# Optimization experiments

Hardware: AMD Instinct MI355X
Metric: run time of the kernel (lower is better)

The kernel has to match this reference:

```python
import jax, jax.numpy as jnp
import numpy as np

NEG_SLOPE = 0.2

def _gat_conv(x, W, att_src, att_dst, bias, src, dst, n_nodes):
    # x: [N, F_in], W: [F_in, F_out], att_*: [F_out], bias: [F_out]
    h = x @ W                                   # [N, F_out]
    a_src = h @ att_src                         # [N]
    a_dst = h @ att_dst                         # [N]
    e = a_src[src] + a_dst[dst]                 # [E]
    e = jnp.where(e > 0, e, NEG_SLOPE * e)      # LeakyReLU
    # segment softmax over incoming edges of each destination node
    m = jax.ops.segment_max(e, dst, num_segments=n_nodes)
    ex = jnp.exp(e - m[dst])
    denom = jax.ops.segment_sum(ex, dst, num_segments=n_nodes)
    alpha = ex / denom[dst]                     # [E]
    msg = alpha[:, None] * h[src]               # [E, F_out]
    out = jax.ops.segment_sum(msg, dst, num_segments=n_nodes)
    return out + bias

def setup_inputs() -> dict:
    key = jax.random.key(0)
    ks = jax.random.split(key, 12)
    N, E, F_in, H, F_out = 50000, 800000, 128, 128, 128
    def glorot(k, shape):
        lim = float(np.sqrt(6.0 / sum(shape))) if len(shape) > 1 else float(np.sqrt(6.0 / shape[0]))
        return jax.random.uniform(k, shape, jnp.float32, -lim, lim)
    return {
        "x": jax.random.normal(ks[0], (N, F_in), jnp.float32),
        "edge_index": jax.random.randint(ks[1], (2, E), 0, N, jnp.int64),
        "W1": glorot(ks[2], (F_in, H)),
        "att_src1": glorot(ks[3], (H,)),
        "att_dst1": glorot(ks[4], (H,)),
        "b1": jnp.zeros((H,), jnp.float32),
        "W2": glorot(ks[5], (H, F_out)),
        "att_src2": glorot(ks[6], (F_out,)),
        "att_dst2": glorot(ks[7], (F_out,)),
        "b2": jnp.zeros((F_out,), jnp.float32),
    }

def reference(x, edge_index, W1, att_src1, att_dst1, b1, W2, att_src2, att_dst2, b2):
    n_nodes = x.shape[0]
    # add self loops (PyG GATConv default)
    loops = jnp.arange(n_nodes, dtype=edge_index.dtype)
    src = jnp.concatenate([edge_index[0], loops])
    dst = jnp.concatenate([edge_index[1], loops])
    h = _gat_conv(x, W1, att_src1, att_dst1, b1, src, dst, n_nodes)
    h = jax.nn.relu(h)
    h = _gat_conv(h, W2, att_src2, att_dst2, b2, src, dst, n_nodes)
    return jax.nn.relu(h)
```

## Files before the change

kernel.cpp:

```cpp
#include <hip/hip_runtime.h>
#include <cstdint>

#define NEG_SLOPE 0.2f
#define F 128

#define BKT_SHIFT 7
#define BKT_SIZE  128
#define NBK_PAD   512
#define CHUNK     4096
#define EPT       8
#define CAP       3072

typedef unsigned short u16;
typedef unsigned int u32;
typedef float float8_t __attribute__((ext_vector_type(8)));
typedef float float4_t __attribute__((ext_vector_type(4)));
typedef short short8_t __attribute__((ext_vector_type(8)));

__device__ inline u16 f2bf(float f) {
    u32 u = __float_as_uint(f);
    u32 r = u + 0x7fffu + ((u >> 16) & 1u);
    return (u16)(r >> 16);
}
__device__ inline float bflo(u32 v) { return __uint_as_float(v << 16); }
__device__ inline float bfhi(u32 v) { return __uint_as_float(v & 0xffff0000u); }

__device__ inline void prep_unit(const float* __restrict__ W, u16* __restrict__ Wt, int u) {
    int frag = u >> 6, lane = u & 63;
    int K0 = frag >> 3, nt = frag & 7;
    int kbase = K0 * 32 + (lane >> 4) * 8;
    int n = nt * 16 + (lane & 15);
    u32 w[4];
    #pragma unroll
    for (int p = 0; p < 4; ++p) {
        u16 e0 = f2bf(W[(size_t)(kbase + 2 * p) * F + n]);
        u16 e1 = f2bf(W[(size_t)(kbase + 2 * p + 1) * F + n]);
        w[p] = (u32)e0 | ((u32)e1 << 16);
    }
    uint4 o; o.x = w[0]; o.y = w[1]; o.z = w[2]; o.w = w[3];
    ((uint4*)Wt)[u] = o;
}

__global__ void __launch_bounds__(512) scatter_prep_kernel(const int* __restrict__ ei, int E, int tot,
                                                           int* __restrict__ bucketCursor,
                                                           u32* __restrict__ pairs,
                                                           const float* __restrict__ W1, u16* __restrict__ Wt1,
                                                           const float* __restrict__ W2, u16* __restrict__ Wt2,
                                                           int nScatBlocks) {
    if ((int)blockIdx.x >= nScatBlocks) {
        int pb = blockIdx.x - nScatBlocks;
        int u = (pb & 3) * 512 + threadIdx.x;
        if (pb < 4) prep_unit(W1, Wt1, u);
        else        prep_unit(W2, Wt2, u);
        return;
    }
    __shared__ int hist[NBK_PAD], excl[NBK_PAD], lcur[NBK_PAD], runb[NBK_PAD];
    __shared__ u32 stage[CHUNK];
    __shared__ u16 bktid[CHUNK];
    int tid = threadIdx.x;
    hist[tid] = 0;
    __syncthreads();
    int base = blockIdx.x * CHUNK;
    int chunkCnt = min(CHUNK, tot - base);
    int rs[EPT], rd[EPT];
    int w = base + tid * EPT;
    if (w + EPT <= E) {
        int4 s0 = *(const int4*)&ei[w];
        int4 s1 = *(const int4*)&ei[w + 4];
        int4 d0 = *(const int4*)&ei[E + w];
        int4 d1 = *(const int4*)&ei[E + w + 4];
        rs[0] = s0.x; rs[1] = s0.y; rs[2] = s0.z; rs[3] = s0.w;
        rs[4] = s1.x; rs[5] = s1.y; rs[6] = s1.z; rs[7] = s1.w;
        rd[0] = d0.x; rd[1] = d0.y; rd[2] = d0.z; rd[3] = d0.w;
        rd[4] = d1.x; rd[5] = d1.y; rd[6] = d1.z; rd[7] = d1.w;
        #pragma unroll
        for (int i = 0; i < EPT; ++i) atomicAdd(&hist[rd[i] >> BKT_SHIFT], 1);
    } else {
        #pragma unroll
        for (int i = 0; i < EPT; ++i) {
            int e = w + i;
            rd[i] = -1;
            if (e < tot) {
                int s, d;
                if (e < E) { s = ei[e]; d = ei[E + e]; } else { s = e - E; d = s; }
                rs[i] = s; rd[i] = d;
                atomicAdd(&hist[d >> BKT_SHIFT], 1);
            }
        }
    }
    __syncthreads();
    int v = hist[tid];
    excl[tid] = v;
    __syncthreads();
    for (int o = 1; o < NBK_PAD; o <<= 1) {
        int u = (tid >= o) ? excl[tid - o] : 0;
        __syncthreads();
        excl[tid] += u;
        __syncthreads();
    }
    int ex = excl[tid] - v;
    __syncthreads();
    excl[tid] = ex;
    lcur[tid] = ex;
    if (v > 0) runb[tid] = tid * CAP + atomicAdd(&bucketCursor[tid], v);
    __syncthreads();
    #pragma unroll
    for (int i = 0; i < EPT; ++i) {
        if (rd[i] >= 0) {
            int b = rd[i] >> BKT_SHIFT;
            int pos = atomicAdd(&lcur[b], 1);
            stage[pos] = ((u32)rs[i] << BKT_SHIFT) | (u32)(rd[i] & (BKT_SIZE - 1));
            bktid[pos] = (u16)b;
        }
    }
    __syncthreads();
    for (int j = tid; j < chunkCnt; j += 512) {
        int b = (int)bktid[j];
        size_t idx = (size_t)runb[b] + (j - excl[b]);
        if (idx < (size_t)(b + 1) * CAP)
            pairs[idx] = stage[j];
    }
}

__global__ void __launch_bounds__(512) bucket_scan_kernel(const int* __restrict__ bucketCursor,
                                                          int* __restrict__ bucketStart) {
    __shared__ int sc[NBK_PAD];
    int t = threadIdx.x;
    int v = min(bucketCursor[t], CAP);
    sc[t] = v;
    __syncthreads();
    for (int o = 1; o < NBK_PAD; o <<= 1) {
        int u = (t >= o) ? sc[t - o] : 0;
        __syncthreads();
        sc[t] += u;
        __syncthreads();
    }
    bucketStart[t] = sc[t] - v;
    if (t == NBK_PAD - 1) bucketStart[NBK_PAD] = sc[t];
}

__device__ void build_body(const u32* __restrict__ pairs, const int* __restrict__ bucketStart,
                           int* __restrict__ row_ptr, int* __restrict__ csr,
                           int N, int tot, int b, char* smem) {
    u32* stage  = (u32*)smem;
    int* sorted = (int*)(smem + CAP * 4);
    int* hist   = (int*)(smem + CAP * 8);
    int* pfx    = (int*)(smem + CAP * 8 + 512);
    int* cur    = (int*)(smem + CAP * 8 + 1024);
    int tid = threadIdx.x;
    size_t srcb = (size_t)b * CAP;
    int dstb = bucketStart[b];
    int cnt = bucketStart[b + 1] - dstb;
    if (tid < BKT_SIZE) hist[tid] = 0;
    __syncthreads();
    for (int j = tid; j < cnt; j += 256) {
        u32 p = pairs[srcb + j];
        stage[j] = p;
        atomicAdd(&hist[p & (BKT_SIZE - 1)], 1);
    }
    __syncthreads();
    if (tid < BKT_SIZE) pfx[tid] = hist[tid];
    __syncthreads();
    for (int o = 1; o < BKT_SIZE; o <<= 1) {
        int u = 0;
        if (tid < BKT_SIZE && tid >= o) u = pfx[tid - o];
        __syncthreads();
        if (tid < BKT_SIZE) pfx[tid] += u;
        __syncthreads();
    }
    if (tid < BKT_SIZE) {
        int ex = pfx[tid] - hist[tid];
        cur[tid] = ex;
        int d = b * BKT_SIZE + tid;
        if (d < N) row_ptr[d] = dstb + ex;
    }
    __syncthreads();
    for (int j = tid; j < cnt; j += 256) {
        u32 p = stage[j];
        int pos = atomicAdd(&cur[p & (BKT_SIZE - 1)], 1);
        sorted[pos] = (int)(p >> BKT_SHIFT);
    }
    __syncthreads();
    for (int j = tid; j < cnt; j += 256) csr[(size_t)dstb + j] = sorted[j];
    if (b == 0 && tid == 0) row_ptr[N] = tot;
}

template<int IN_BF16>
__device__ void gemm_body(const void* __restrict__ in, const u16* __restrict__ Wt,
                          const float* __restrict__ att_s, const float* __restrict__ att_d,
                          u16* __restrict__ h, float* __restrict__ asrc, float* __restrict__ adst,
                          int N, int gblk, u16* wlds) {
    int tid = threadIdx.x;
    {
        const uint4* src = (const uint4*)Wt;
        uint4* dst = (uint4*)wlds;
        #pragma unroll
        for (int i = 0; i < 8; ++i) dst[tid + i * 256] = src[tid + i * 256];
    }
    __syncthreads();
    int wave = tid >> 6, lane = tid & 63;
    int li = lane & 15, grp = lane >> 4;
    int rowBase = (gblk * 4 + wave) * 16;
    if (rowBase >= N) return;
    int row = rowBase + li;
    if (row > N - 1) row = N - 1;

    short8_t b[4];
    if (IN_BF16) {
        const u16* xp = (const u16*)in + (size_t)row * F + grp * 8;
        #pragma unroll
        for (int K0 = 0; K0 < 4; ++K0)
            b[K0] = *(const short8_t*)(xp + K0 * 32);
    } else {
        const float* xp = (const float*)in + (size_t)row * F + grp * 8;
        #pragma unroll
        for (int K0 = 0; K0 < 4; ++K0) {
            float8_t xv = *(const float8_t*)(xp + K0 * 32);
            short8_t t;
            #pragma unroll
            for (int i = 0; i < 8; ++i) t[i] = (short)f2bf(xv[i]);
            b[K0] = t;
        }
    }

    float4_t acc[8];
    #pragma unroll
    for (int nt = 0; nt < 8; ++nt) acc[nt] = (float4_t){0.f, 0.f, 0.f, 0.f};
    #pragma unroll
    for (int nt = 0; nt < 8; ++nt) {
        #pragma unroll
        for (int K0 = 0; K0 < 4; ++K0) {
            short8_t a = *(const short8_t*)&wlds[((K0 * 8 + nt) * 64 + lane) * 8];
            acc[nt] = __builtin_amdgcn_mfma_f32_16x16x32_bf16(a, b[K0], acc[nt], 0, 0, 0);
        }
    }

    u16* hr = h + (size_t)row * F + grp * 4;
    #pragma unroll
    for (int nt = 0; nt < 8; ++nt) {
        u32 lo = (u32)f2bf(acc[nt][0]) | ((u32)f2bf(acc[nt][1]) << 16);
        u32 hi = (u32)f2bf(acc[nt][2]) | ((u32)f2bf(acc[nt][3]) << 16);
        uint2 st; st.x = lo; st.y = hi;
        *(uint2*)(hr + (size_t)nt * 16) = st;
    }

    float rs = 0.f, rd = 0.f;
    #pragma unroll
    for (int nt = 0; nt < 8; ++nt) {
        float4 a4 = *(const float4*)(att_s + nt * 16 + grp * 4);
        float4 d4 = *(const float4*)(att_d + nt * 16 + grp * 4);
        rs += acc[nt][0] * a4.x + acc[nt][1] * a4.y + acc[nt][2] * a4.z + acc[nt][3] * a4.w;
        rd += acc[nt][0] * d4.x + acc[nt][1] * d4.y + acc[nt][2] * d4.z + acc[nt][3] * d4.w;
    }
    rs += __shfl_xor(rs, 16); rs += __shfl_xor(rs, 32);
    rd += __shfl_xor(rd, 16); rd += __shfl_xor(rd, 32);
    if (grp == 0) { asrc[row] = rs; adst[row] = rd; }
}

template<int IN_BF16>
__global__ void __launch_bounds__(256) gemm_mfma_kernel(const void* __restrict__ in,
    const u16* __restrict__ Wt, const float* __restrict__ att_s, const float* __restrict__ att_d,
    u16* __restrict__ h, float* __restrict__ asrc, float* __restrict__ adst, int N)
{
    __shared__ u16 wlds[16384];
    gemm_body<IN_BF16>(in, Wt, att_s, att_d, h, asrc, adst, N, blockIdx.x, wlds);
}

__global__ void __launch_bounds__(256) build_gemm_kernel(
    const u32* __restrict__ pairs, const int* __restrict__ bucketStart,
    int* __restrict__ row_ptr, int* __restrict__ csr, int N, int tot,
    const float* __restrict__ x, const u16* __restrict__ Wt,
    const float* __restrict__ att_s, const float* __restrict__ att_d,
    u16* __restrict__ h, float* __restrict__ asrc, float* __restrict__ adst, int NBK)
{
    __shared__ __align__(16) char smem[32768];
    if ((int)blockIdx.x < NBK) {
        build_body(pairs, bucketStart, row_ptr, csr, N, tot, blockIdx.x, smem);
    } else {
        gemm_body<0>(x, Wt, att_s, att_d, h, asrc, adst, N, blockIdx.x - NBK, (u16*)smem);
    }
}

template<int U>
__device__ __forceinline__ void gfma(const uint4* __restrict__ h4, int lane, int s, float p, int t,
                                     float (&acc)[8]) {
    int ss[U]; float pp[U]; uint4 vv[U];
    #pragma unroll
    for (int i = 0; i < U; ++i) { ss[i] = __shfl(s, t + i, 16); pp[i] = __shfl(p, t + i, 16); }
    #pragma unroll
    for (int i = 0; i < U; ++i) vv[i] = h4[(size_t)ss[i] * 16 + lane];
    #pragma unroll
    for (int i = 0; i < U; ++i) {
        acc[0] = fmaf(pp[i], bflo(vv[i].x), acc[0]);
        acc[1] = fmaf(pp[i], bfhi(vv[i].x), acc[1]);
        acc[2] = fmaf(pp[i], bflo(vv[i].y), acc[2]);
        acc[3] = fmaf(pp[i], bfhi(vv[i].y), acc[3]);
        acc[4] = fmaf(pp[i], bflo(vv[i].z), acc[4]);
        acc[5] = fmaf(pp[i], bfhi(vv[i].z), acc[5]);
        acc[6] = fmaf(pp[i], bflo(vv[i].w), acc[6]);
        acc[7] = fmaf(pp[i], bfhi(vv[i].w), acc[7]);
    }
}

template<int OUT_BF16>
__global__ void __launch_bounds__(256) aggregate_kernel(
    const u16* __restrict__ h, const float* __restrict__ asrc, const float* __restrict__ adst,
    const int* __restrict__ row_ptr, const int* __restrict__ csr,
    const float* __restrict__ bias, void* __restrict__ out, int N)
{
    int gid = blockIdx.x * 16 + (threadIdx.x >> 4);
    if (gid >= N) return;
    int lane = threadIdx.x & 15;
    int start = row_ptr[gid];
    int deg = row_ptr[gid + 1] - start;
    float ad = adst[gid];

    const uint4* h4 = (const uint4*)h;
    float denom = 0.f;
    float acc[8] = {0.f, 0.f, 0.f, 0.f, 0.f, 0.f, 0.f, 0.f};

    int c0 = 0;
    int cnt = min(16, deg);
    int s = 0; float a = 0.f;
    if (lane < cnt) { s = csr[start + lane]; a = asrc[s]; }
    for (;;) {
        float p = 0.f;
        if (lane < cnt) {
            float e = a + ad;
            e = (e > 0.f) ? e : NEG_SLOPE * e;
            p = __expf(fminf(e, 70.f));
        }
        denom += p;

        int nc0 = c0 + 16;
        int ncnt = min(16, deg - nc0);
        int s2 = 0; float a2 = 0.f;
        if (nc0 < deg && lane < ncnt) { s2 = csr[start + nc0 + lane]; a2 = asrc[s2]; }

        int t = 0;
        for (; t + 8 <= cnt; t += 8) gfma<8>(h4, lane, s, p, t, acc);
        for (; t + 4 <= cnt; t += 4) gfma<4>(h4, lane, s, p, t, acc);
        for (; t < cnt; ++t)         gfma<1>(h4, lane, s, p, t, acc);

        if (nc0 >= deg) break;
        c0 = nc0; cnt = ncnt; s = s2; a = a2;
    }

    #pragma unroll
    for (int o = 1; o < 16; o <<= 1) denom += __shfl_xor(denom, o);
    float inv = 1.0f / denom;
    const float* bp = bias + lane * 8;
    float r[8];
    #pragma unroll
    for (int j = 0; j < 8; ++j) {
        float v = fmaf(acc[j], inv, bp[j]);
        r[j] = v > 0.f ? v : 0.f;
    }
    if (OUT_BF16) {
        u32 w[4];
        #pragma unroll
        for (int p2 = 0; p2 < 4; ++p2)
            w[p2] = (u32)f2bf(r[2 * p2]) | ((u32)f2bf(r[2 * p2 + 1]) << 16);
        uint4 st; st.x = w[0]; st.y = w[1]; st.z = w[2]; st.w = w[3];
        ((uint4*)out)[(size_t)gid * 16 + lane] = st;
    } else {
        float4 o0 = make_float4(r[0], r[1], r[2], r[3]);
        float4 o1 = make_float4(r[4], r[5], r[6], r[7]);
        ((float4*)out)[(size_t)gid * 32 + lane * 2]     = o0;
        ((float4*)out)[(size_t)gid * 32 + lane * 2 + 1] = o1;
    }
}

static inline size_t align_up(size_t v, size_t a) { return (v + a - 1) & ~(a - 1); }

extern "C" void kernel_launch(void* const* d_in, const int* in_sizes, int n_in,
                              void* d_out, int out_size, void* d_ws, size_t ws_size,
                              hipStream_t stream) {
    const float* x   = (const float*)d_in[0];
    const int*   ei  = (const int*)d_in[1];
    const float* W1  = (const float*)d_in[2];
    const float* as1 = (const float*)d_in[3];
    const float* ad1 = (const float*)d_in[4];
    const float* b1  = (const float*)d_in[5];
    const float* W2  = (const float*)d_in[6];
    const float* as2 = (const float*)d_in[7];
    const float* ad2 = (const float*)d_in[8];
    const float* b2  = (const float*)d_in[9];

    int N = in_sizes[0] / F;
    int E = in_sizes[1] / 2;
    int tot = E + N;

    char* ws = (char*)d_ws;
    size_t off = 0;
    #define ALLOC(type, name, count)                                    \
        type* name = (type*)(ws + off);                                  \
        off = align_up(off + (size_t)(count) * sizeof(type), 256);
    ALLOC(u16,   h,       (size_t)N * F);
    ALLOC(u16,   out1,    (size_t)N * F);
    ALLOC(float, asrc,    N);
    ALLOC(float, adst,    N);
    ALLOC(int,   row_ptr, N + 4);
    ALLOC(int,   csr,     tot);
    ALLOC(u32,   pairs,   (size_t)NBK_PAD * CAP);
    ALLOC(int,   bucketStart,  NBK_PAD + 1);
    ALLOC(int,   bucketCursor, NBK_PAD);
    ALLOC(u16,   Wt1,     16384);
    ALLOC(u16,   Wt2,     16384);
    #undef ALLOC

    hipMemsetAsync(bucketCursor, 0, NBK_PAD * sizeof(int), stream);

    int NBK = (N + BKT_SIZE - 1) / BKT_SIZE;
    int nchunks = (tot + CHUNK - 1) / CHUNK;
    int ngemm = (N + 63) / 64;
    int nagg  = (N + 15) / 16;

    scatter_prep_kernel<<<nchunks + 8, 512, 0, stream>>>(ei, E, tot, bucketCursor, pairs,
                                                         W1, Wt1, W2, Wt2, nchunks);
    bucket_scan_kernel<<<1, NBK_PAD, 0, stream>>>(bucketCursor, bucketStart);
    build_gemm_kernel<<<NBK + ngemm, 256, 0, stream>>>(pairs, bucketStart, row_ptr, csr, N, tot,
                                                       x, Wt1, as1, ad1, h, asrc, adst, NBK);
    aggregate_kernel<1><<<nagg, 256, 0, stream>>>(h, asrc, adst, row_ptr, csr, b1, out1, N);
    gemm_mfma_kernel<1><<<ngemm, 256, 0, stream>>>(out1, Wt2, as2, ad2, h, asrc, adst, N);
    aggregate_kernel<0><<<nagg, 256, 0, stream>>>(h, asrc, adst, row_ptr, csr, b2, d_out, N);
}
```

Before: 201.2 us.

## Fuse layer-1 aggregation with layer-2 GEMM and use shuffle-based block scans

Merges the first-layer aggregation with the second-layer projection. Each 16-node block writes its aggregated bf16 rows to LDS, then runs MFMA against Wt2 and computes the attention dot products, so the intermediate out1 round trip through global memory and one kernel launch go away. Separate h2/asrc2/adst2 buffers are added so layer-1 data is not overwritten while other blocks still read it. The 512-element block scans in the scatter and bucket-scan kernels are replaced with a wave-shuffle scan plus per-wave sums, which cuts the number of barriers. The fused kernel has no gid>=N guard (fine here since N is a multiple of 16) and loads Wt2 from global per wave instead of staging it in LDS.

```diff
diff --git a/kernel.cpp b/kernel.cpp
--- a/kernel.cpp
+++ b/kernel.cpp
@@ -39,6 +39,21 @@
     }
     uint4 o; o.x = w[0]; o.y = w[1]; o.z = w[2]; o.w = w[3];
     ((uint4*)Wt)[u] = o;
+}
+
+__device__ inline int block_excl_scan_512(int v, int tid, int* wsum) {
+    int incl = v;
+    #pragma unroll
+    for (int o = 1; o < 64; o <<= 1) {
+        int u = __shfl_up(incl, o);
+        if ((tid & 63) >= o) incl += u;
+    }
+    if ((tid & 63) == 63) wsum[tid >> 6] = incl;
+    __syncthreads();
+    int woff = 0;
+    #pragma unroll
+    for (int w0 = 0; w0 < 7; ++w0) woff += (w0 < (tid >> 6)) ? wsum[w0] : 0;
+    return woff + incl - v;
 }
 
 __global__ void __launch_bounds__(512) scatter_prep_kernel(const int* __restrict__ ei, int E, int tot,
@@ -55,6 +70,7 @@
         return;
     }
     __shared__ int hist[NBK_PAD], excl[NBK_PAD], lcur[NBK_PAD], runb[NBK_PAD];
+    __shared__ int wsum[8];
     __shared__ u32 stage[CHUNK];
     __shared__ u16 bktid[CHUNK];
     int tid = threadIdx.x;
@@ -90,16 +106,7 @@
     }
     __syncthreads();
     int v = hist[tid];
-    excl[tid] = v;
-    __syncthreads();
-    for (int o = 1; o < NBK_PAD; o <<= 1) {
-        int u = (tid >= o) ? excl[tid - o] : 0;
-        __syncthreads();
-        excl[tid] += u;
-        __syncthreads();
-    }
-    int ex = excl[tid] - v;
-    __syncthreads();
+    int ex = block_excl_scan_512(v, tid, wsum);
     excl[tid] = ex;
     lcur[tid] = ex;
     if (v > 0) runb[tid] = tid * CAP + atomicAdd(&bucketCursor[tid], v);
@@ -124,19 +131,12 @@
 
 __global__ void __launch_bounds__(512) bucket_scan_kernel(const int* __restrict__ bucketCursor,
                                                           int* __restrict__ bucketStart) {
-    __shared__ int sc[NBK_PAD];
+    __shared__ int wsum[8];
     int t = threadIdx.x;
     int v = min(bucketCursor[t], CAP);
-    sc[t] = v;
-    __syncthreads();
-    for (int o = 1; o < NBK_PAD; o <<= 1) {
-        int u = (t >= o) ? sc[t - o] : 0;
-        __syncthreads();
-        sc[t] += u;
-        __syncthreads();
-    }
-    bucketStart[t] = sc[t] - v;
-    if (t == NBK_PAD - 1) bucketStart[NBK_PAD] = sc[t];
+    int ex = block_excl_scan_512(v, t, wsum);
+    bucketStart[t] = ex;
+    if (t == NBK_PAD - 1) bucketStart[NBK_PAD] = ex + v;
 }
 
 __device__ void build_body(const u32* __restrict__ pairs, const int* __restrict__ bucketStart,
@@ -257,15 +257,6 @@
     if (grp == 0) { asrc[row] = rs; adst[row] = rd; }
 }
 
-template<int IN_BF16>
-__global__ void __launch_bounds__(256) gemm_mfma_kernel(const void* __restrict__ in,
-    const u16* __restrict__ Wt, const float* __restrict__ att_s, const float* __restrict__ att_d,
-    u16* __restrict__ h, float* __restrict__ asrc, float* __restrict__ adst, int N)
-{
-    __shared__ u16 wlds[16384];
-    gemm_body<IN_BF16>(in, Wt, att_s, att_d, h, asrc, adst, N, blockIdx.x, wlds);
-}
-
 __global__ void __launch_bounds__(256) build_gemm_kernel(
     const u32* __restrict__ pairs, const int* __restrict__ bucketStart,
     int* __restrict__ row_ptr, int* __restrict__ csr, int N, int tot,
@@ -302,23 +293,11 @@
     }
 }
 
-template<int OUT_BF16>
-__global__ void __launch_bounds__(256) aggregate_kernel(
-    const u16* __restrict__ h, const float* __restrict__ asrc, const float* __restrict__ adst,
-    const int* __restrict__ row_ptr, const int* __restrict__ csr,
-    const float* __restrict__ bias, void* __restrict__ out, int N)
-{
-    int gid = blockIdx.x * 16 + (threadIdx.x >> 4);
-    if (gid >= N) return;
-    int lane = threadIdx.x & 15;
-    int start = row_ptr[gid];
-    int deg = row_ptr[gid + 1] - start;
-    float ad = adst[gid];
-
+__device__ __forceinline__ float agg_core(
+    const u16* __restrict__ h, const float* __restrict__ asrc, float ad,
+    int start, int deg, const int* __restrict__ csr, int lane, float (&acc)[8]) {
     const uint4* h4 = (const uint4*)h;
     float denom = 0.f;
-    float acc[8] = {0.f, 0.f, 0.f, 0.f, 0.f, 0.f, 0.f, 0.f};
-
     int c0 = 0;
     int cnt = min(16, deg);
     int s = 0; float a = 0.f;
@@ -345,9 +324,98 @@
         if (nc0 >= deg) break;
         c0 = nc0; cnt = ncnt; s = s2; a = a2;
     }
-
     #pragma unroll
     for (int o = 1; o < 16; o <<= 1) denom += __shfl_xor(denom, o);
+    return denom;
+}
+
+#define OL_STRIDE 136
+__global__ void __launch_bounds__(256) agg_gemm_kernel(
+    const u16* __restrict__ h, const float* __restrict__ asrc, const float* __restrict__ adst,
+    const int* __restrict__ row_ptr, const int* __restrict__ csr,
+    const float* __restrict__ bias,
+    const u16* __restrict__ Wt2, const float* __restrict__ att_s2, const float* __restrict__ att_d2,
+    u16* __restrict__ h2, float* __restrict__ asrc2, float* __restrict__ adst2, int N)
+{
+    __shared__ u16 out_lds[16 * OL_STRIDE];
+    __shared__ float sdots[2][4][16];
+    int tid = threadIdx.x;
+    int gidBase = blockIdx.x * 16;
+    int gid = gidBase + (tid >> 4);
+    int lane = tid & 15;
+
+    int start = row_ptr[gid];
+    int deg = row_ptr[gid + 1] - start;
+    float acc[8] = {0.f, 0.f, 0.f, 0.f, 0.f, 0.f, 0.f, 0.f};
+    float denom = agg_core(h, asrc, adst[gid], start, deg, csr, lane, acc);
+    float inv = 1.0f / denom;
+    const float* bp = bias + lane * 8;
+    u32 wpk[4];
+    #pragma unroll
+    for (int p2 = 0; p2 < 4; ++p2) {
+        float v0 = fmaf(acc[2 * p2],     inv, bp[2 * p2]);
+        float v1 = fmaf(acc[2 * p2 + 1], inv, bp[2 * p2 + 1]);
+        v0 = v0 > 0.f ? v0 : 0.f;
+        v1 = v1 > 0.f ? v1 : 0.f;
+        wpk[p2] = (u32)f2bf(v0) | ((u32)f2bf(v1) << 16);
+    }
+    {
+        uint4 st; st.x = wpk[0]; st.y = wpk[1]; st.z = wpk[2]; st.w = wpk[3];
+        *(uint4*)&out_lds[(tid >> 4) * OL_STRIDE + lane * 8] = st;
+    }
+    __syncthreads();
+
+    int l = tid & 63, wv = tid >> 6;
+    int li = l & 15, grp = l >> 4;
+    short8_t b[4];
+    #pragma unroll
+    for (int K0 = 0; K0 < 4; ++K0)
+        b[K0] = *(const short8_t*)&out_lds[li * OL_STRIDE + grp * 8 + K0 * 32];
+
+    float rs = 0.f, rd = 0.f;
+    #pragma unroll
+    for (int q = 0; q < 2; ++q) {
+        int nt = wv * 2 + q;
+        float4_t acc2 = (float4_t){0.f, 0.f, 0.f, 0.f};
+        #pragma unroll
+        for (int K0 = 0; K0 < 4; ++K0) {
+            short8_t a = *(const short8_t*)&Wt2[((K0 * 8 + nt) * 64 + l) * 8];
+            acc2 = __builtin_amdgcn_mfma_f32_16x16x32_bf16(a, b[K0], acc2, 0, 0, 0);
+        }
+        int row = gidBase + li;
+        u32 lo = (u32)f2bf(acc2[0]) | ((u32)f2bf(acc2[1]) << 16);
+        u32 hi = (u32)f2bf(acc2[2]) | ((u32)f2bf(acc2[3]) << 16);
+        uint2 st; st.x = lo; st.y = hi;
+        *(uint2*)(h2 + (size_t)row * F + nt * 16 + grp * 4) = st;
+        float4 a4 = *(const float4*)(att_s2 + nt * 16 + grp * 4);
+        float4 d4 = *(const float4*)(att_d2 + nt * 16 + grp * 4);
+        rs += acc2[0] * a4.x + acc2[1] * a4.y + acc2[2] * a4.z + acc2[3] * a4.w;
+        rd += acc2[0] * d4.x + acc2[1] * d4.y + acc2[2] * d4.z + acc2[3] * d4.w;
+    }
+    rs += __shfl_xor(rs, 16); rs += __shfl_xor(rs, 32);
+    rd += __shfl_xor(rd, 16); rd += __shfl_xor(rd, 32);
+    if (grp == 0) { sdots[0][wv][li] = rs; sdots[1][wv][li] = rd; }
+    __syncthreads();
+    if (tid < 16) {
+        float s = sdots[0][0][tid] + sdots[0][1][tid] + sdots[0][2][tid] + sdots[0][3][tid];
+        float d = sdots[1][0][tid] + sdots[1][1][tid] + sdots[1][2][tid] + sdots[1][3][tid];
+        asrc2[gidBase + tid] = s;
+        adst2[gidBase + tid] = d;
+    }
+}
+
+__global__ void __launch_bounds__(256) aggregate_out_kernel(
+    const u16* __restrict__ h, const float* __restrict__ asrc, const float* __restrict__ adst,
+    const int* __restrict__ row_ptr, const int* __restrict__ csr,
+    const float* __restrict__ bias, float* __restrict__ out, int N)
+{
+    int gid = blockIdx.x * 16 + (threadIdx.x >> 4);
+    if (gid >= N) return;
+    int lane = threadIdx.x & 15;
+    int start = row_ptr[gid];
+    int deg = row_ptr[gid + 1] - start;
+    float acc[8] = {0.f, 0.f, 0.f, 0.f, 0.f, 0.f, 0.f, 0.f};
+    float denom = agg_core(h, asrc, adst[gid], start, deg, csr, lane, acc);
     float inv = 1.0f / denom;
     const float* bp = bias + lane * 8;
     float r[8];
@@ -356,19 +424,10 @@
         float v = fmaf(acc[j], inv, bp[j]);
         r[j] = v > 0.f ? v : 0.f;
     }
-    if (OUT_BF16) {
-        u32 w[4];
-        #pragma unroll
-        for (int p2 = 0; p2 < 4; ++p2)
-            w[p2] = (u32)f2bf(r[2 * p2]) | ((u32)f2bf(r[2 * p2 + 1]) << 16);
-        uint4 st; st.x = w[0]; st.y = w[1]; st.z = w[2]; st.w = w[3];
-        ((uint4*)out)[(size_t)gid * 16 + lane] = st;
-    } else {
-        float4 o0 = make_float4(r[0], r[1], r[2], r[3]);
-        float4 o1 = make_float4(r[4], r[5], r[6], r[7]);
-        ((float4*)out)[(size_t)gid * 32 + lane * 2]     = o0;
-        ((float4*)out)[(size_t)gid * 32 + lane * 2 + 1] = o1;
-    }
+    float4 o0 = make_float4(r[0], r[1], r[2], r[3]);
+    float4 o1 = make_float4(r[4], r[5], r[6], r[7]);
+    ((float4*)out)[(size_t)gid * 32 + lane * 2]     = o0;
+    ((float4*)out)[(size_t)gid * 32 + lane * 2 + 1] = o1;
 }
 
 static inline size_t align_up(size_t v, size_t a) { return (v + a - 1) & ~(a - 1); }
@@ -397,9 +456,11 @@
         type* name = (type*)(ws + off);                                  \
         off = align_up(off + (size_t)(count) * sizeof(type), 256);
     ALLOC(u16,   h,       (size_t)N * F);
-    ALLOC(u16,   out1,    (size_t)N * F);
+    ALLOC(u16,   h2,      (size_t)N * F);
     ALLOC(float, asrc,    N);
     ALLOC(float, adst,    N);
+    ALLOC(float, asrc2,   N);
+    ALLOC(float, adst2,   N);
     ALLOC(int,   row_ptr, N + 4);
     ALLOC(int,   csr,     tot);
     ALLOC(u32,   pairs,   (size_t)NBK_PAD * CAP);
@@ -421,7 +482,8 @@
     bucket_scan_kernel<<<1, NBK_PAD, 0, stream>>>(bucketCursor, bucketStart);
     build_gemm_kernel<<<NBK + ngemm, 256, 0, stream>>>(pairs, bucketStart, row_ptr, csr, N, tot,
                                                        x, Wt1, as1, ad1, h, asrc, adst, NBK);
-    aggregate_kernel<1><<<nagg, 256, 0, stream>>>(h, asrc, adst, row_ptr, csr, b1, out1, N);
-    gemm_mfma_kernel<1><<<ngemm, 256, 0, stream>>>(out1, Wt2, as2, ad2, h, asrc, adst, N);
-    aggregate_kernel<0><<<nagg, 256, 0, stream>>>(h, asrc, adst, row_ptr, csr, b2, d_out, N);
-}
+    agg_gemm_kernel<<<nagg, 256, 0, stream>>>(h, asrc, adst, row_ptr, csr, b1,
+                                              Wt2, as2, ad2, h2, asrc2, adst2, N);
+    aggregate_out_kernel<<<nagg, 256, 0, stream>>>(h2, asrc2, adst2, row_ptr, csr, b2,
+                                                   (float*)d_out, N);
+}
```

Result: faster. 191.8 us (-4.7%).
